# Kernel optimization log

Hardware: AMD Instinct MI355X
Metric: run time of the kernel (lower is better)

The kernel has to match this reference:

```python
import jax, jax.numpy as jnp
import numpy as np


def setup_inputs() -> dict:
    key = jax.random.key(0)
    ks = jax.random.split(key, 9)
    B, S, E, H, D = 8, 1000, 1024, 16, 64
    sc = 0.02
    return {
        "x": jax.random.normal(ks[0], (B, S, E), dtype=jnp.float32),
        "wq": jax.random.normal(ks[1], (H, E, D), dtype=jnp.float32) * sc,
        "bq": jax.random.normal(ks[2], (H, D), dtype=jnp.float32) * sc,
        "wk": jax.random.normal(ks[3], (H, E, D), dtype=jnp.float32) * sc,
        "bk": jax.random.normal(ks[4], (H, D), dtype=jnp.float32) * sc,
        "wv": jax.random.normal(ks[5], (H, E, D), dtype=jnp.float32) * sc,
        "bv": jax.random.normal(ks[6], (H, D), dtype=jnp.float32) * sc,
        "wp": jax.random.normal(ks[7], (E, E), dtype=jnp.float32) * sc,
        "bp": jax.random.normal(ks[8], (E,), dtype=jnp.float32) * sc,
    }


def reference(x, wq, bq, wk, bk, wv, bv, wp, bp):
    B, S, E = x.shape
    H, _, D = wq.shape
    # per-head projections, all heads batched: [B,H,S,D]
    q = jnp.einsum('bse,hed->bhsd', x, wq) + bq[None, :, None, :]
    k = jnp.einsum('bse,hed->bhsd', x, wk) + bk[None, :, None, :]
    v = jnp.einsum('bse,hed->bhsd', x, wv) + bv[None, :, None, :]
    # NOTE: original scales by sqrt(seq_len), not sqrt(head_dim)
    scores = jnp.einsum('bhsd,bhtd->bhst', q, k) / jnp.asarray(S, x.dtype) ** 0.5
    causal = jnp.tril(jnp.ones((S, S), dtype=bool))  # mask[:S,:S] == 1 keeps
    scores = jnp.where(causal, scores, jnp.asarray(-jnp.inf, x.dtype))
    attn = jax.nn.softmax(scores, axis=-1)
    z = jnp.einsum('bhst,bhtd->bhsd', attn, v)
    # concat heads in head order -> [B,S,E]
    y = z.transpose(0, 2, 1, 3).reshape(B, S, E)
    # projection then exact GELU (dropout is identity at eval)
    return jax.nn.gelu(jnp.einsum('bse,ef->bsf', y, wp) + bp, approximate=False)
```

## Files before the change

### kernel.cpp

```cpp
#include <hip/hip_runtime.h>
#include <hip/hip_bf16.h>
#include <math.h>

constexpr int B_ = 8, S_ = 1000, E_ = 1024, H_ = 16, D_ = 64;
constexpr int M_ = B_ * S_;

using bf16x8 = __attribute__((ext_vector_type(8))) __bf16;
using u16x8  = __attribute__((ext_vector_type(8))) unsigned short;
using f32x4  = __attribute__((ext_vector_type(4))) float;

static __device__ __forceinline__ unsigned short f2bf(float f) {
    union { float f; unsigned u; } c; c.f = f;
    return (unsigned short)((c.u + 0x7FFF + ((c.u >> 16) & 1)) >> 16);
}
static __device__ __forceinline__ unsigned short f2bf_fast(float f) {
    union { float f; unsigned u; } c; c.f = f;
    return (unsigned short)((c.u + 0x8000) >> 16);
}
static __device__ __forceinline__ float bfr2f(unsigned short s) {
    union { unsigned u; float f; } c; c.u = ((unsigned)s) << 16;
    return c.f;
}

static __device__ __forceinline__ void gld16(const unsigned short* g, unsigned short* lds) {
    __builtin_amdgcn_global_load_lds(
        (__attribute__((address_space(1))) void*)(g),
        (__attribute__((address_space(3))) void*)(lds), 16, 0, 0);
}

__global__ __launch_bounds__(256) void cast_x_kernel(
    const float* __restrict__ x, unsigned short* __restrict__ xbf)
{
    const size_t i = ((size_t)blockIdx.x * 256 + threadIdx.x) * 4;
    float4 v = *(const float4*)(x + i);
    ushort4 o;
    o.x = f2bf(v.x); o.y = f2bf(v.y); o.z = f2bf(v.z); o.w = f2bf(v.w);
    *(ushort4*)(xbf + i) = o;
}

__global__ __launch_bounds__(256) void transpose_wqkv_kernel(
    const float* __restrict__ wq, const float* __restrict__ wk,
    const float* __restrict__ wv, unsigned short* __restrict__ WT)
{
    __shared__ unsigned short Ts[64 * 65];
    const int et = blockIdx.x, zh = blockIdx.y;
    const int z = zh >> 4, h = zh & 15;
    const float* src = (z == 0 ? wq : z == 1 ? wk : wv) + (size_t)h * E_ * D_;

    const int d = threadIdx.x & 63;
    const int e0 = threadIdx.x >> 6;
    #pragma unroll
    for (int p = 0; p < 16; ++p) {
        const int e = e0 + p * 4;
        Ts[d * 65 + e] = f2bf(src[(size_t)(et * 64 + e) * D_ + d]);
    }
    __syncthreads();
    const int e = threadIdx.x & 63;
    const int d0 = threadIdx.x >> 6;
    #pragma unroll
    for (int p = 0; p < 16; ++p) {
        const int dd = d0 + p * 4;
        WT[((size_t)zh * 64 + dd) * E_ + et * 64 + e] = Ts[dd * 65 + e];
    }
}

__global__ __launch_bounds__(256) void transpose_wp_kernel(
    const float* __restrict__ wp, unsigned short* __restrict__ wpT)
{
    __shared__ unsigned short Ts[64 * 65];
    const int et = blockIdx.x, ft = blockIdx.y;
    const int f = threadIdx.x & 63;
    const int e0 = threadIdx.x >> 6;
    #pragma unroll
    for (int p = 0; p < 16; ++p) {
        const int e = e0 + p * 4;
        Ts[f * 65 + e] = f2bf(wp[(size_t)(et * 64 + e) * E_ + ft * 64 + f]);
    }
    __syncthreads();
    const int e = threadIdx.x & 63;
    const int f0 = threadIdx.x >> 6;
    #pragma unroll
    for (int p = 0; p < 16; ++p) {
        const int ff = f0 + p * 4;
        wpT[((size_t)(ft * 64 + ff)) * E_ + et * 64 + e] = Ts[ff * 65 + e];
    }
}

__global__ __launch_bounds__(256) void transpose_v_kernel(
    const unsigned short* __restrict__ vb, unsigned short* __restrict__ vt)
{
    __shared__ unsigned short Ts[64 * 65];
    const int st = blockIdx.x, bh = blockIdx.y;
    const size_t ibase = (size_t)bh * S_ * D_;
    const size_t obase = (size_t)bh * D_ * S_;

    const int d = threadIdx.x & 63;
    const int s0 = threadIdx.x >> 6;
    #pragma unroll
    for (int p = 0; p < 16; ++p) {
        const int s = s0 + p * 4;
        const int srow = st * 64 + s;
        Ts[s * 65 + d] = (srow < S_) ? vb[ibase + (size_t)srow * D_ + d] : 0;
    }
    __syncthreads();
    const int s = threadIdx.x & 63;
    const int d0 = threadIdx.x >> 6;
    const int scol = st * 64 + s;
    if (scol < S_) {
        #pragma unroll
        for (int p = 0; p < 16; ++p) {
            const int dd = d0 + p * 4;
            vt[obase + (size_t)dd * S_ + scol] = Ts[s * 65 + dd];
        }
    }
}

__global__ __launch_bounds__(256) void qkv_mfma_kernel(
    const unsigned short* __restrict__ xbf, const unsigned short* __restrict__ WT,
    const float* __restrict__ bq, const float* __restrict__ bk,
    const float* __restrict__ bv,
    unsigned short* __restrict__ qb, unsigned short* __restrict__ kb,
    unsigned short* __restrict__ vb)
{
    __shared__ unsigned short As[128 * 64];
    __shared__ unsigned short Bs[128 * 64];

    const int tid  = threadIdx.x;
    const int wave = tid >> 6, lane = tid & 63;
    const int m16  = lane & 15, quad = lane >> 4;
    const int wm   = wave >> 1, wn = wave & 1;
    const int n0   = blockIdx.x * 128;
    const int m0   = blockIdx.y * 128;

    f32x4 acc[4][4];
    #pragma unroll
    for (int nf = 0; nf < 4; ++nf)
        #pragma unroll
        for (int mf = 0; mf < 4; ++mf)
            acc[nf][mf] = (f32x4){0.f, 0.f, 0.f, 0.f};

    const int lrow = lane >> 3;
    const int lcol = (lane & 7) << 3;

    int a_srow[4];
    #pragma unroll
    for (int j = 0; j < 4; ++j) {
        int r = m0 + (wave * 4 + j) * 8 + lrow;
        a_srow[j] = (r < M_) ? r : (M_ - 1);
    }

    for (int kk = 0; kk < E_; kk += 64) {
        __syncthreads();
        #pragma unroll
        for (int j = 0; j < 4; ++j) {
            const int i = wave * 4 + j;
            gld16(xbf + (size_t)a_srow[j] * E_ + kk + lcol, &As[i * 512]);
            gld16(WT + (size_t)(n0 + i * 8 + lrow) * E_ + kk + lcol, &Bs[i * 512]);
        }
        __syncthreads();

        #pragma unroll
        for (int kh = 0; kh < 2; ++kh) {
            const int ko = kh * 32 + quad * 8;
            bf16x8 af[4];
            #pragma unroll
            for (int mf = 0; mf < 4; ++mf)
                af[mf] = *(const bf16x8*)&As[(wm * 64 + mf * 16 + m16) * 64 + ko];
            #pragma unroll
            for (int nf = 0; nf < 4; ++nf) {
                const bf16x8 bfr = *(const bf16x8*)&Bs[(wn * 64 + nf * 16 + m16) * 64 + ko];
                #pragma unroll
                for (int mf = 0; mf < 4; ++mf)
                    acc[nf][mf] = __builtin_amdgcn_mfma_f32_16x16x32_bf16(
                        af[mf], bfr, acc[nf][mf], 0, 0, 0);
            }
        }
    }

    const int z = n0 >> 10;
    const int h = ((n0 >> 6) + wn) & 15;
    unsigned short* const ob = (z == 0) ? qb : (z == 1) ? kb : vb;
    const float* const bz    = (z == 0) ? bq : (z == 1) ? bk : bv;

    float biasv[4];
    #pragma unroll
    for (int nf = 0; nf < 4; ++nf)
        biasv[nf] = bz[h * D_ + nf * 16 + m16];

    #pragma unroll
    for (int mf = 0; mf < 4; ++mf)
        #pragma unroll
        for (int r = 0; r < 4; ++r) {
            const int row = m0 + wm * 64 + mf * 16 + quad * 4 + r;
            if (row < M_) {
                const int b = row / S_, s = row % S_;
                const size_t obase = (((size_t)b * H_ + h) * S_ + s) * D_ + m16;
                #pragma unroll
                for (int nf = 0; nf < 4; ++nf)
                    ob[obase + nf * 16] = f2bf(acc[nf][mf][r] + biasv[nf]);
            }
        }
}

__global__ __launch_bounds__(256) void attn_flash_kernel(
    const unsigned short* __restrict__ q, const unsigned short* __restrict__ k,
    const unsigned short* __restrict__ vt, unsigned short* __restrict__ ybf)
{
    constexpr int P_ = 72;
    __shared__ unsigned short Qs[64 * P_];
    __shared__ unsigned short Ks[64 * P_];
    __shared__ unsigned short Vt[64 * P_];
    __shared__ unsigned short Ps[4][16 * P_];

    const int tid  = threadIdx.x;
    const int wave = tid >> 6, lane = tid & 63;
    const int m16  = lane & 15, quad = lane >> 4;
    const int qt = (int)gridDim.x - 1 - (int)blockIdx.x;
    const int h = blockIdx.y, b = blockIdx.z;
    const size_t bh  = ((size_t)b * H_ + h) * S_;
    const size_t vtb = ((size_t)b * H_ + h) * (size_t)D_ * S_;
    const float sl2e = 0.031622776601683794f * 1.4426950408889634f;

    const int c8 = (tid & 7) * 8;
    const int r0 = tid >> 3;

    #pragma unroll
    for (int rr = 0; rr < 64; rr += 32) {
        const int r = r0 + rr;
        const int srow = qt * 64 + r;
        u16x8 val = {0, 0, 0, 0, 0, 0, 0, 0};
        if (srow < S_) val = *(const u16x8*)(q + (bh + srow) * D_ + c8);
        u16x8 o;
        #pragma unroll
        for (int j = 0; j < 8; ++j) o[j] = f2bf_fast(bfr2f(val[j]) * sl2e);
        *(u16x8*)&Qs[r * P_ + c8] = o;
    }
    __syncthreads();

    const bf16x8 qa0 = *(const bf16x8*)&Qs[(wave * 16 + m16) * P_ + quad * 8];
    const bf16x8 qa1 = *(const bf16x8*)&Qs[(wave * 16 + m16) * P_ + 32 + quad * 8];

    f32x4 O[4] = {{0,0,0,0},{0,0,0,0},{0,0,0,0},{0,0,0,0}};
    float l_i[4] = {0.f, 0.f, 0.f, 0.f};

    const int qrow_base = qt * 64 + wave * 16 + quad * 4;

    u16x8 kreg[2], vreg[2];
    #pragma unroll
    for (int i = 0; i < 2; ++i) {
        const int srow = r0 + i * 32;
        kreg[i] = *(const u16x8*)(k + (bh + srow) * D_ + c8);
        vreg[i] = *(const u16x8*)(vt + vtb + (size_t)(r0 + i * 32) * S_ + c8);
    }

    for (int tt = 0; tt <= qt; ++tt) {
        const int t0 = tt * 64;
        __syncthreads();
        #pragma unroll
        for (int i = 0; i < 2; ++i) {
            *(u16x8*)&Ks[(r0 + i * 32) * P_ + c8] = kreg[i];
            *(u16x8*)&Vt[(r0 + i * 32) * P_ + c8] = vreg[i];
        }
        __syncthreads();

        if (tt < qt) {
            const int nt0 = t0 + 64;
            #pragma unroll
            for (int i = 0; i < 2; ++i) {
                const int t = r0 + i * 32;
                const int srow = nt0 + t;
                u16x8 kv = {0,0,0,0,0,0,0,0}, vv = {0,0,0,0,0,0,0,0};
                if (srow < S_) kv = *(const u16x8*)(k + (bh + srow) * D_ + c8);
                if (nt0 + c8 < S_)
                    vv = *(const u16x8*)(vt + vtb + (size_t)t * S_ + nt0 + c8);
                kreg[i] = kv; vreg[i] = vv;
            }
        }

        f32x4 sc[4];
        #pragma unroll
        for (int ts = 0; ts < 4; ++ts) {
            const bf16x8 kb0 = *(const bf16x8*)&Ks[(ts * 16 + m16) * P_ + quad * 8];
            const bf16x8 kb1 = *(const bf16x8*)&Ks[(ts * 16 + m16) * P_ + 32 + quad * 8];
            f32x4 a = {0.f, 0.f, 0.f, 0.f};
            a = __builtin_amdgcn_mfma_f32_16x16x32_bf16(qa0, kb0, a, 0, 0, 0);
            a = __builtin_amdgcn_mfma_f32_16x16x32_bf16(qa1, kb1, a, 0, 0, 0);
            sc[ts] = a;
        }

        unsigned short* const pw = &Ps[wave][0];
        if (tt == qt) {
            #pragma unroll
            for (int ts = 0; ts < 4; ++ts) {
                const int t = t0 + ts * 16 + m16;
                #pragma unroll
                for (int r = 0; r < 4; ++r) {
                    float p = __builtin_amdgcn_exp2f(sc[ts][r]);
                    p = (t <= qrow_base + r) ? p : 0.f;
                    pw[(quad * 4 + r) * P_ + ts * 16 + m16] = f2bf_fast(p);
                    l_i[r] += p;
                }
            }
        } else {
            #pragma unroll
            for (int ts = 0; ts < 4; ++ts)
                #pragma unroll
                for (int r = 0; r < 4; ++r) {
                    const float p = __builtin_amdgcn_exp2f(sc[ts][r]);
                    pw[(quad * 4 + r) * P_ + ts * 16 + m16] = f2bf_fast(p);
                    l_i[r] += p;
                }
        }

        const bf16x8 pa0 = *(const bf16x8*)&pw[m16 * P_ + quad * 8];
        const bf16x8 pa1 = *(const bf16x8*)&pw[m16 * P_ + 32 + quad * 8];
        #pragma unroll
        for (int db = 0; db < 4; ++db) {
            const bf16x8 vb0 = *(const bf16x8*)&Vt[(db * 16 + m16) * P_ + quad * 8];
            const bf16x8 vb1 = *(const bf16x8*)&Vt[(db * 16 + m16) * P_ + 32 + quad * 8];
            O[db] = __builtin_amdgcn_mfma_f32_16x16x32_bf16(pa0, vb0, O[db], 0, 0, 0);
            O[db] = __builtin_amdgcn_mfma_f32_16x16x32_bf16(pa1, vb1, O[db], 0, 0, 0);
        }
    }

    #pragma unroll
    for (int off = 1; off < 16; off <<= 1)
        #pragma unroll
        for (int r = 0; r < 4; ++r)
            l_i[r] += __shfl_xor(l_i[r], off, 64);

    #pragma unroll
    for (int r = 0; r < 4; ++r) {
        const int qrow = qrow_base + r;
        if (qrow < S_) {
            const float invl = 1.0f / l_i[r];
            #pragma unroll
            for (int db = 0; db < 4; ++db)
                ybf[((size_t)b * S_ + qrow) * E_ + h * D_ + db * 16 + m16] =
                    f2bf(O[db][r] * invl);
        }
    }
}

__global__ __launch_bounds__(256) void proj_mfma_kernel(
    const unsigned short* __restrict__ ybf, const unsigned short* __restrict__ wpT,
    const float* __restrict__ bp, float* __restrict__ out)
{
    constexpr int P = 72;
    __shared__ unsigned short As[128 * P];
    __shared__ unsigned short Bs[128 * P];

    const int tid = threadIdx.x;
    const int wave = tid >> 6, lane = tid & 63;
    const int m16 = lane & 15, quad = lane >> 4;
    const int wm = wave >> 1, wn = wave & 1;
    const int m0 = blockIdx.x * 128;
    const int n0 = blockIdx.y * 128;

    f32x4 acc[4][4];
    #pragma unroll
    for (int nf = 0; nf < 4; ++nf)
        #pragma unroll
        for (int mf = 0; mf < 4; ++mf)
            acc[nf][mf] = (f32x4){0.f, 0.f, 0.f, 0.f};

    const int ar = tid & 31;
    const int ac8 = (tid >> 5) * 8;

    int asrow[4];
    #pragma unroll
    for (int p = 0; p < 4; ++p) {
        int r = m0 + ar + p * 32;
        asrow[p] = (r < M_) ? r : (M_ - 1);
    }

    u16x8 areg[4], breg[4];
    #pragma unroll
    for (int p = 0; p < 4; ++p) {
        areg[p] = *(const u16x8*)(ybf + (size_t)asrow[p] * E_ + ac8);
        breg[p] = *(const u16x8*)(wpT + (size_t)(n0 + ar + p * 32) * E_ + ac8);
    }

    for (int kk = 0; kk < E_; kk += 64) {
        __syncthreads();
        #pragma unroll
        for (int p = 0; p < 4; ++p) {
            *(u16x8*)&As[(ar + p * 32) * P + ac8] = areg[p];
            *(u16x8*)&Bs[(ar + p * 32) * P + ac8] = breg[p];
        }
        __syncthreads();

        if (kk + 64 < E_) {
            const int kn = kk + 64;
            #pragma unroll
            for (int p = 0; p < 4; ++p) {
                areg[p] = *(const u16x8*)(ybf + (size_t)asrow[p] * E_ + kn + ac8);
                breg[p] = *(const u16x8*)(wpT + (size_t)(n0 + ar + p * 32) * E_ + kn + ac8);
            }
        }

        #pragma unroll
        for (int kh = 0; kh < 2; ++kh) {
            const int ko = kh * 32 + quad * 8;
            bf16x8 af[4];
            #pragma unroll
            for (int mf = 0; mf < 4; ++mf)
                af[mf] = *(const bf16x8*)&As[(wm * 64 + mf * 16 + m16) * P + ko];
            #pragma unroll
            for (int nf = 0; nf < 4; ++nf) {
                const bf16x8 bfr = *(const bf16x8*)&Bs[(wn * 64 + nf * 16 + m16) * P + ko];
                #pragma unroll
                for (int mf = 0; mf < 4; ++mf)
                    acc[nf][mf] = __builtin_amdgcn_mfma_f32_16x16x32_bf16(
                        af[mf], bfr, acc[nf][mf], 0, 0, 0);
            }
        }
    }

    float biasv[4];
    #pragma unroll
    for (int nf = 0; nf < 4; ++nf)
        biasv[nf] = bp[n0 + wn * 64 + nf * 16 + m16];

    #pragma unroll
    for (int mf = 0; mf < 4; ++mf)
        #pragma unroll
        for (int r = 0; r < 4; ++r) {
            const int row = m0 + wm * 64 + mf * 16 + quad * 4 + r;
            if (row < M_) {
                #pragma unroll
                for (int nf = 0; nf < 4; ++nf) {
                    const int col = n0 + wn * 64 + nf * 16 + m16;
                    const float t = acc[nf][mf][r] + biasv[nf];
                    const float g = 0.5f * t * (1.0f + erff(t * 0.70710678118654752f));
                    out[(size_t)row * E_ + col] = g;
                }
            }
        }
}

extern "C" void kernel_launch(void* const* d_in, const int* in_sizes, int n_in,
                              void* d_out, int out_size, void* d_ws, size_t ws_size,
                              hipStream_t stream)
{
    const float* x  = (const float*)d_in[0];
    const float* wq = (const float*)d_in[1];
    const float* bq = (const float*)d_in[2];
    const float* wk = (const float*)d_in[3];
    const float* bk = (const float*)d_in[4];
    const float* wv = (const float*)d_in[5];
    const float* bv = (const float*)d_in[6];
    const float* wp = (const float*)d_in[7];
    const float* bp = (const float*)d_in[8];
    float* out = (float*)d_out;

    const size_t nME = (size_t)M_ * E_;
    unsigned short* xbf = (unsigned short*)d_ws;
    unsigned short* WT  = xbf + nME;
    unsigned short* wpT = WT + 3145728;
    unsigned short* qb  = wpT + 1048576;
    unsigned short* kb  = qb + nME;
    unsigned short* vb  = kb + nME;
    unsigned short* ybf = vb + nME;
    unsigned short* vtr = ybf + nME;

    cast_x_kernel<<<dim3((unsigned)(nME / 1024)), 256, 0, stream>>>(x, xbf);
    transpose_wqkv_kernel<<<dim3(16, 48), 256, 0, stream>>>(wq, wk, wv, WT);
    transpose_wp_kernel<<<dim3(16, 16), 256, 0, stream>>>(wp, wpT);

    qkv_mfma_kernel<<<dim3(3072 / 128, (M_ + 127) / 128), 256, 0, stream>>>(
        xbf, WT, bq, bk, bv, qb, kb, vb);
    transpose_v_kernel<<<dim3(16, B_ * H_), 256, 0, stream>>>(vb, vtr);
    attn_flash_kernel<<<dim3((S_ + 63) / 64, H_, B_), 256, 0, stream>>>(
        qb, kb, vtr, ybf);
    proj_mfma_kernel<<<dim3((M_ + 127) / 128, E_ / 128), 256, 0, stream>>>(
        ybf, wpT, bp, out);
}
```

Measured before the change: 302.5 us.

## Double-buffer LDS with async global-to-LDS loads and remap blocks for locality in GEMMs

The QKV and projection GEMM kernels now use double-buffered shared memory, issuing direct global-to-LDS loads for the next K tile while MFMAs run on the current one, with a single barrier per iteration. The projection kernel drops its register-staged padded layout and uses the same gld16 path as the QKV kernel. Both kernels also remap the flat block index, grouping blocks in strides of eight, apparently to improve cache reuse of tiles across concurrently running blocks. Doubling LDS per block may lower occupancy, the unpadded layout may raise bank conflicts in the projection kernel, and the remap hardcodes the grid shape.

```diff
diff --git a/kernel.cpp b/kernel.cpp
--- a/kernel.cpp
+++ b/kernel.cpp
@@ -122,15 +122,18 @@
     unsigned short* __restrict__ qb, unsigned short* __restrict__ kb,
     unsigned short* __restrict__ vb)
 {
-    __shared__ unsigned short As[128 * 64];
-    __shared__ unsigned short Bs[128 * 64];
+    __shared__ unsigned short As[2][128 * 64];
+    __shared__ unsigned short Bs[2][128 * 64];
 
     const int tid  = threadIdx.x;
     const int wave = tid >> 6, lane = tid & 63;
     const int m16  = lane & 15, quad = lane >> 4;
     const int wm   = wave >> 1, wn = wave & 1;
-    const int n0   = blockIdx.x * 128;
-    const int m0   = blockIdx.y * 128;
+
+    const int f  = (int)(blockIdx.y * gridDim.x + blockIdx.x);
+    const int fp = (f & 7) * 189 + (f >> 3);
+    const int n0 = (fp % 24) * 128;
+    const int m0 = (fp / 24) * 128;
 
     f32x4 acc[4][4];
     #pragma unroll
@@ -143,21 +146,33 @@
     const int lcol = (lane & 7) << 3;
 
     int a_srow[4];
+    int b_srow[4];
     #pragma unroll
     for (int j = 0; j < 4; ++j) {
         int r = m0 + (wave * 4 + j) * 8 + lrow;
         a_srow[j] = (r < M_) ? r : (M_ - 1);
-    }
-
-    for (int kk = 0; kk < E_; kk += 64) {
-        __syncthreads();
-        #pragma unroll
-        for (int j = 0; j < 4; ++j) {
-            const int i = wave * 4 + j;
-            gld16(xbf + (size_t)a_srow[j] * E_ + kk + lcol, &As[i * 512]);
-            gld16(WT + (size_t)(n0 + i * 8 + lrow) * E_ + kk + lcol, &Bs[i * 512]);
-        }
-        __syncthreads();
+        b_srow[j] = n0 + (wave * 4 + j) * 8 + lrow;
+    }
+
+    #pragma unroll
+    for (int j = 0; j < 4; ++j) {
+        const int i = wave * 4 + j;
+        gld16(xbf + (size_t)a_srow[j] * E_ + lcol, &As[0][i * 512]);
+        gld16(WT + (size_t)b_srow[j] * E_ + lcol, &Bs[0][i * 512]);
+    }
+    __syncthreads();
+
+    int cur = 0;
+    for (int kt = 0; kt < 16; ++kt) {
+        if (kt < 15) {
+            const int kn = (kt + 1) * 64;
+            #pragma unroll
+            for (int j = 0; j < 4; ++j) {
+                const int i = wave * 4 + j;
+                gld16(xbf + (size_t)a_srow[j] * E_ + kn + lcol, &As[cur ^ 1][i * 512]);
+                gld16(WT + (size_t)b_srow[j] * E_ + kn + lcol, &Bs[cur ^ 1][i * 512]);
+            }
+        }
 
         #pragma unroll
         for (int kh = 0; kh < 2; ++kh) {
@@ -165,16 +180,19 @@
             bf16x8 af[4];
             #pragma unroll
             for (int mf = 0; mf < 4; ++mf)
-                af[mf] = *(const bf16x8*)&As[(wm * 64 + mf * 16 + m16) * 64 + ko];
+                af[mf] = *(const bf16x8*)&As[cur][(wm * 64 + mf * 16 + m16) * 64 + ko];
             #pragma unroll
             for (int nf = 0; nf < 4; ++nf) {
-                const bf16x8 bfr = *(const bf16x8*)&Bs[(wn * 64 + nf * 16 + m16) * 64 + ko];
+                const bf16x8 bfr = *(const bf16x8*)&Bs[cur][(wn * 64 + nf * 16 + m16) * 64 + ko];
                 #pragma unroll
                 for (int mf = 0; mf < 4; ++mf)
                     acc[nf][mf] = __builtin_amdgcn_mfma_f32_16x16x32_bf16(
                         af[mf], bfr, acc[nf][mf], 0, 0, 0);
             }
         }
+
+        __syncthreads();
+        cur ^= 1;
     }
 
     const int z = n0 >> 10;
@@ -346,16 +364,18 @@
     const unsigned short* __restrict__ ybf, const unsigned short* __restrict__ wpT,
     const float* __restrict__ bp, float* __restrict__ out)
 {
-    constexpr int P = 72;
-    __shared__ unsigned short As[128 * P];
-    __shared__ unsigned short Bs[128 * P];
+    __shared__ unsigned short As[2][128 * 64];
+    __shared__ unsigned short Bs[2][128 * 64];
 
     const int tid = threadIdx.x;
     const int wave = tid >> 6, lane = tid & 63;
     const int m16 = lane & 15, quad = lane >> 4;
     const int wm = wave >> 1, wn = wave & 1;
-    const int m0 = blockIdx.x * 128;
-    const int n0 = blockIdx.y * 128;
+
+    const int f  = (int)(blockIdx.y * gridDim.x + blockIdx.x);
+    const int fp = (f & 7) * 63 + (f >> 3);
+    const int m0 = (fp % 63) * 128;
+    const int n0 = (fp / 63) * 128;
 
     f32x4 acc[4][4];
     #pragma unroll
@@ -364,38 +384,35 @@
         for (int mf = 0; mf < 4; ++mf)
             acc[nf][mf] = (f32x4){0.f, 0.f, 0.f, 0.f};
 
-    const int ar = tid & 31;
-    const int ac8 = (tid >> 5) * 8;
-
-    int asrow[4];
-    #pragma unroll
-    for (int p = 0; p < 4; ++p) {
-        int r = m0 + ar + p * 32;
-        asrow[p] = (r < M_) ? r : (M_ - 1);
-    }
-
-    u16x8 areg[4], breg[4];
-    #pragma unroll
-    for (int p = 0; p < 4; ++p) {
-        areg[p] = *(const u16x8*)(ybf + (size_t)asrow[p] * E_ + ac8);
-        breg[p] = *(const u16x8*)(wpT + (size_t)(n0 + ar + p * 32) * E_ + ac8);
-    }
-
-    for (int kk = 0; kk < E_; kk += 64) {
-        __syncthreads();
-        #pragma unroll
-        for (int p = 0; p < 4; ++p) {
-            *(u16x8*)&As[(ar + p * 32) * P + ac8] = areg[p];
-            *(u16x8*)&Bs[(ar + p * 32) * P + ac8] = breg[p];
-        }
-        __syncthreads();
-
-        if (kk + 64 < E_) {
-            const int kn = kk + 64;
-            #pragma unroll
-            for (int p = 0; p < 4; ++p) {
-                areg[p] = *(const u16x8*)(ybf + (size_t)asrow[p] * E_ + kn + ac8);
-                breg[p] = *(const u16x8*)(wpT + (size_t)(n0 + ar + p * 32) * E_ + kn + ac8);
+    const int lrow = lane >> 3;
+    const int lcol = (lane & 7) << 3;
+
+    int a_srow[4];
+    int b_srow[4];
+    #pragma unroll
+    for (int j = 0; j < 4; ++j) {
+        int r = m0 + (wave * 4 + j) * 8 + lrow;
+        a_srow[j] = (r < M_) ? r : (M_ - 1);
+        b_srow[j] = n0 + (wave * 4 + j) * 8 + lrow;
+    }
+
+    #pragma unroll
+    for (int j = 0; j < 4; ++j) {
+        const int i = wave * 4 + j;
+        gld16(ybf + (size_t)a_srow[j] * E_ + lcol, &As[0][i * 512]);
+        gld16(wpT + (size_t)b_srow[j] * E_ + lcol, &Bs[0][i * 512]);
+    }
+    __syncthreads();
+
+    int cur = 0;
+    for (int kt = 0; kt < 16; ++kt) {
+        if (kt < 15) {
+            const int kn = (kt + 1) * 64;
+            #pragma unroll
+            for (int j = 0; j < 4; ++j) {
+                const int i = wave * 4 + j;
+                gld16(ybf + (size_t)a_srow[j] * E_ + kn + lcol, &As[cur ^ 1][i * 512]);
+                gld16(wpT + (size_t)b_srow[j] * E_ + kn + lcol, &Bs[cur ^ 1][i * 512]);
             }
         }
 
@@ -405,16 +422,19 @@
             bf16x8 af[4];
             #pragma unroll
             for (int mf = 0; mf < 4; ++mf)
-                af[mf] = *(const bf16x8*)&As[(wm * 64 + mf * 16 + m16) * P + ko];
+                af[mf] = *(const bf16x8*)&As[cur][(wm * 64 + mf * 16 + m16) * 64 + ko];
             #pragma unroll
             for (int nf = 0; nf < 4; ++nf) {
-                const bf16x8 bfr = *(const bf16x8*)&Bs[(wn * 64 + nf * 16 + m16) * P + ko];
+                const bf16x8 bfr = *(const bf16x8*)&Bs[cur][(wn * 64 + nf * 16 + m16) * 64 + ko];
                 #pragma unroll
                 for (int mf = 0; mf < 4; ++mf)
                     acc[nf][mf] = __builtin_amdgcn_mfma_f32_16x16x32_bf16(
                         af[mf], bfr, acc[nf][mf], 0, 0, 0);
             }
         }
+
+        __syncthreads();
+        cur ^= 1;
     }
 
     float biasv[4];
```

Result: slower. 316.1 us (+4.5%).
